# Optimization experiments

Measured on AMD Instinct MI355X. Metric: run time of the kernel, lower is better.

The kernel has to match this reference:

```python
import jax, jax.numpy as jnp
import numpy as np

N_SRC = 200000
N_DST = 50000
N_EDGES = 800000
IN_FEATS = 128
OUT_FEATS = 64


def setup_inputs() -> dict:
    key = jax.random.key(0)
    k1, k2, k3, k4 = jax.random.split(key, 4)
    x = jax.random.normal(k1, (N_SRC, IN_FEATS), dtype=jnp.float32)
    edge_src = jax.random.randint(k2, (N_EDGES,), 0, N_SRC, dtype=jnp.int64)
    edge_dst = jax.random.randint(k3, (N_EDGES,), 0, N_DST, dtype=jnp.int64)
    W = jax.random.normal(k4, (IN_FEATS, OUT_FEATS), dtype=jnp.float32) / np.sqrt(IN_FEATS)
    b = jnp.zeros((OUT_FEATS,), dtype=jnp.float32)
    return {"x": x, "edge_src": edge_src, "edge_dst": edge_dst, "W": W, "b": b, "n_dst": N_DST}


def reference(x, edge_src, edge_dst, W, b, n_dst):
    # DGL SAGEConv, aggregator_type='gcn'.
    # lin_before_mp = in_feats > out_feats (128 > 64) -> project before aggregation.
    h_src = x @ W                      # [n_src, out]
    h_dst = h_src[:n_dst]              # dst nodes are the first n_dst src nodes
    # sparse gather + segment reduce (SpMM): sum of projected neighbor feats per dst
    msgs = h_src[edge_src]             # [n_edges, out]
    neigh_sum = jax.ops.segment_sum(msgs, edge_dst, num_segments=n_dst)
    deg = jax.ops.segment_sum(jnp.ones_like(edge_dst, dtype=h_src.dtype),
                              edge_dst, num_segments=n_dst)  # in-degree per dst
    h = (neigh_sum + h_dst) / (deg + 1.0)[:, None]
    return h + b
```

## Files before the change

### kernel.cpp

```cpp
#include <hip/hip_runtime.h>
#include <hip/hip_bf16.h>

#define IN_F   128
#define OUT_F  64
#define CAP    96
#define NGB    512

typedef __attribute__((ext_vector_type(8))) short short8;
typedef __attribute__((ext_vector_type(4))) float floatx4;

__device__ inline unsigned short f32_to_bf16_rne(float f) {
    unsigned int u = __float_as_uint(f);
    unsigned int r = (u + 0x7FFFu + ((u >> 16) & 1u)) >> 16;
    return (unsigned short)r;
}
__device__ inline float bf16_to_f32(unsigned short u) {
    return __uint_as_float((unsigned int)u << 16);
}
__device__ inline unsigned int cvt_pk_bf16(float lo, float hi) {
    unsigned int r;
    asm volatile("v_cvt_pk_bf16_f32 %0, %1, %2" : "=v"(r) : "v"(lo), "v"(hi));
    return r;
}
__device__ __forceinline__ void async_copy16(const float* gsrc, float* ldst) {
    __builtin_amdgcn_global_load_lds(
        (const __attribute__((address_space(1))) unsigned int*)(const void*)gsrc,
        (__attribute__((address_space(3))) unsigned int*)(void*)ldst,
        16, 0, 0);
}

__global__ __launch_bounds__(256) void prep_w(const float* __restrict__ W,
                                              unsigned short* __restrict__ Wtg) {
    const int o = blockIdx.x * 256 + threadIdx.x;
    #pragma unroll
    for (int m = 0; m < 4; ++m) {
        const int idx = o + m * 2048;
        const int f = idx >> 9, r = idx & 511, l = r >> 3, j = r & 7;
        const int t = f >> 2, s = f & 3;
        const int k = 32 * s + 8 * (l >> 4) + j;
        const int c = 16 * t + (l & 15);
        Wtg[idx] = f32_to_bf16_rne(W[k * 64 + c]);
    }
}

__global__ __launch_bounds__(256) void bin_edges(const int* __restrict__ esrc,
                                                 const int* __restrict__ edst,
                                                 int* __restrict__ cnt,
                                                 int* __restrict__ elist,
                                                 int n_edges) {
    const int e = blockIdx.x * 256 + threadIdx.x;
    if (e < n_edges) {
        const int d = edst[e];
        const int slot = atomicAdd(&cnt[d], 1);
        if (slot < CAP) elist[(size_t)d * CAP + slot] = esrc[e];
    }
}

__global__ __launch_bounds__(256, 2) void gemm_xw(const float* __restrict__ x,
                                                  const unsigned short* __restrict__ Wtg,
                                                  unsigned short* __restrict__ h,
                                                  int nTiles) {
    __shared__ float xs[2][64 * 128];

    const int tid = threadIdx.x;
    const int lane = tid & 63;
    const int wave = tid >> 6;
    const int lrow = lane & 15;
    const int lkg  = lane >> 4;
    const int rx   = lrow & 7;

    short8 bf[4][4];
    #pragma unroll
    for (int f = 0; f < 16; ++f)
        (&bf[0][0])[f] = *reinterpret_cast<const short8*>(&Wtg[(f * 64 + lane) * 8]);
    asm volatile("s_waitcnt vmcnt(0)" ::: "memory");

    auto stage = [&](int buf, int tile) {
        const float* xt = x + (size_t)tile * 64 * IN_F;
        #pragma unroll
        for (int i = 0; i < 8; ++i) {
            const int j = (wave * 8 + i) * 64 + lane;
            const int row = j >> 5;
            const int c16 = (j & 31) ^ (row & 7);
            const float* src = xt + row * 128 + c16 * 4;
            float* dst = &xs[buf][(wave * 8 + i) * 256];
            async_copy16(src, dst);
        }
    };

    int cur = 0;
    int tile = blockIdx.x;
    if (tile < nTiles) stage(0, tile);

    for (; tile < nTiles; tile += NGB) {
        const int next = tile + NGB;
        if (next < nTiles) {
            stage(cur ^ 1, next);
            asm volatile("s_waitcnt vmcnt(8)" ::: "memory");
        } else {
            asm volatile("s_waitcnt vmcnt(0)" ::: "memory");
        }
        __builtin_amdgcn_sched_barrier(0);
        __builtin_amdgcn_s_barrier();

        const float* xt = &xs[cur][0];
        const int row = 16 * wave + lrow;
        short8 a[4];
        #pragma unroll
        for (int s = 0; s < 4; ++s) {
            const int ca = (8 * s + 2 * lkg) ^ rx;
            const int cb = (8 * s + 2 * lkg + 1) ^ rx;
            const float4 va = *reinterpret_cast<const float4*>(&xt[row * 128 + ca * 4]);
            const float4 vb = *reinterpret_cast<const float4*>(&xt[row * 128 + cb * 4]);
            union { unsigned int u[4]; short8 v; } cv;
            cv.u[0] = cvt_pk_bf16(va.x, va.y);
            cv.u[1] = cvt_pk_bf16(va.z, va.w);
            cv.u[2] = cvt_pk_bf16(vb.x, vb.y);
            cv.u[3] = cvt_pk_bf16(vb.z, vb.w);
            a[s] = cv.v;
        }

        floatx4 acc[4];
        #pragma unroll
        for (int t = 0; t < 4; ++t) acc[t] = (floatx4){0.f, 0.f, 0.f, 0.f};
        #pragma unroll
        for (int t = 0; t < 4; ++t)
            #pragma unroll
            for (int s = 0; s < 4; ++s)
                acc[t] = __builtin_amdgcn_mfma_f32_16x16x32_bf16(a[s], bf[t][s], acc[t], 0, 0, 0);

        unsigned short* hb = h + ((size_t)tile * 64 + 16 * wave) * OUT_F;
        #pragma unroll
        for (int t = 0; t < 4; ++t)
            #pragma unroll
            for (int r = 0; r < 4; ++r)
                hb[(size_t)(4 * lkg + r) * OUT_F + 16 * t + lrow] =
                    f32_to_bf16_rne(acc[t][r]);

        __builtin_amdgcn_s_barrier();
        cur ^= 1;
    }
}

__global__ __launch_bounds__(256) void gather_finalize(const unsigned short* __restrict__ h,
                                                       const int* __restrict__ cnt,
                                                       const int* __restrict__ elist,
                                                       const float* __restrict__ b,
                                                       float* __restrict__ out,
                                                       int n_dst) {
    const int lane = threadIdx.x & 63;
    const int d = blockIdx.x * 4 + (threadIdx.x >> 6);
    if (d >= n_dst) return;

    const int eq = lane >> 4;
    const int p  = lane & 15;

    const int cnt_d = cnt[d];
    const int m = min(cnt_d, CAP);
    const size_t ebase = (size_t)d * CAP;

    float4 acc = {0.f, 0.f, 0.f, 0.f};

    for (int base = 0; base < m; base += 64) {
        const int lim = min(64, m - base);
        const int sidx = (base + lane < m) ? elist[ebase + base + lane] : 0;
        for (int j = 0; j < lim; j += 4) {
            const int myj = j + eq;
            const bool valid = myj < lim;
            const int s = __shfl(sidx, valid ? myj : 0);
            const ushort4 v = *reinterpret_cast<const ushort4*>(&h[(size_t)s * OUT_F + 4 * p]);
            const float w = valid ? 1.0f : 0.0f;
            acc.x += w * bf16_to_f32(v.x);
            acc.y += w * bf16_to_f32(v.y);
            acc.z += w * bf16_to_f32(v.z);
            acc.w += w * bf16_to_f32(v.w);
        }
    }

    acc.x += __shfl_xor(acc.x, 32); acc.y += __shfl_xor(acc.y, 32);
    acc.z += __shfl_xor(acc.z, 32); acc.w += __shfl_xor(acc.w, 32);
    acc.x += __shfl_xor(acc.x, 16); acc.y += __shfl_xor(acc.y, 16);
    acc.z += __shfl_xor(acc.z, 16); acc.w += __shfl_xor(acc.w, 16);

    if (lane < 16) {
        const ushort4 hd = *reinterpret_cast<const ushort4*>(&h[(size_t)d * OUT_F + 4 * p]);
        const float4 bb = *reinterpret_cast<const float4*>(&b[4 * p]);
        const float inv = 1.0f / ((float)cnt_d + 1.0f);
        float4 o;
        o.x = (acc.x + bf16_to_f32(hd.x)) * inv + bb.x;
        o.y = (acc.y + bf16_to_f32(hd.y)) * inv + bb.y;
        o.z = (acc.z + bf16_to_f32(hd.z)) * inv + bb.z;
        o.w = (acc.w + bf16_to_f32(hd.w)) * inv + bb.w;
        *reinterpret_cast<float4*>(&out[(size_t)d * OUT_F + 4 * p]) = o;
    }
}

static inline size_t align256(size_t v) { return (v + 255) & ~(size_t)255; }

extern "C" void kernel_launch(void* const* d_in, const int* in_sizes, int n_in,
                              void* d_out, int out_size, void* d_ws, size_t ws_size,
                              hipStream_t stream) {
    const float* x    = (const float*)d_in[0];
    const int*   esrc = (const int*)d_in[1];
    const int*   edst = (const int*)d_in[2];
    const float* W    = (const float*)d_in[3];
    const float* b    = (const float*)d_in[4];

    const int n_rows  = in_sizes[0] / IN_F;
    const int n_edges = in_sizes[1];
    const int n_dst   = out_size / OUT_F;
    float* out = (float*)d_out;

    const size_t hBytes  = (size_t)n_rows * OUT_F * sizeof(unsigned short);
    const size_t cntOff  = align256(hBytes);
    const size_t elOff   = align256(cntOff + (size_t)n_dst * 4);
    const size_t wtOff   = align256(elOff + (size_t)n_dst * CAP * 4);
    const size_t needed  = wtOff + (size_t)IN_F * OUT_F * sizeof(unsigned short);

    unsigned short* h = (unsigned short*)d_ws;

    if (ws_size >= needed) {
        int* cnt             = (int*)((char*)d_ws + cntOff);
        int* elist           = (int*)((char*)d_ws + elOff);
        unsigned short* Wtg  = (unsigned short*)((char*)d_ws + wtOff);

        hipMemsetAsync(cnt, 0, (size_t)n_dst * 4, stream);

        prep_w<<<8, 256, 0, stream>>>(W, Wtg);

        const int eBlocks = (n_edges + 255) / 256;
        bin_edges<<<eBlocks, 256, 0, stream>>>(esrc, edst, cnt, elist, n_edges);

        const int nTiles = n_rows / 64;
        gemm_xw<<<NGB, 256, 0, stream>>>(x, Wtg, h, nTiles);

        const int gBlocks = (n_dst + 3) / 4;
        gather_finalize<<<gBlocks, 256, 0, stream>>>(h, cnt, elist, b, out, n_dst);
    } else {
        hipMemsetAsync(out, 0, (size_t)out_size * sizeof(float), stream);
    }
}
```

Measured before the change: 108.4 us.

## Fuse edge binning into GEMM kernel and split counters into front/back halves

Removes the separate bin_edges launch by running edge binning in a grid-stride loop at the end of the persistent GEMM kernel. Edges are split by parity into two counters that fill the per-destination slot list from the front and from the back, which halves contention on each atomic counter. The gather kernel reads the two ranges and uses the summed counts for the degree. The cost is a second counter array, and the binning still runs after each block's GEMM tiles rather than overlapping with them. The per-half cap of 48 can drop edges that the single cap of 96 would have kept when the two halves are uneven.

```diff
diff --git a/kernel.cpp b/kernel.cpp
--- a/kernel.cpp
+++ b/kernel.cpp
@@ -4,6 +4,7 @@
 #define IN_F   128
 #define OUT_F  64
 #define CAP    96
+#define HCAP   48
 #define NGB    512
 
 typedef __attribute__((ext_vector_type(8))) short short8;
@@ -43,23 +44,16 @@
     }
 }
 
-__global__ __launch_bounds__(256) void bin_edges(const int* __restrict__ esrc,
-                                                 const int* __restrict__ edst,
-                                                 int* __restrict__ cnt,
-                                                 int* __restrict__ elist,
-                                                 int n_edges) {
-    const int e = blockIdx.x * 256 + threadIdx.x;
-    if (e < n_edges) {
-        const int d = edst[e];
-        const int slot = atomicAdd(&cnt[d], 1);
-        if (slot < CAP) elist[(size_t)d * CAP + slot] = esrc[e];
-    }
-}
-
-__global__ __launch_bounds__(256, 2) void gemm_xw(const float* __restrict__ x,
-                                                  const unsigned short* __restrict__ Wtg,
-                                                  unsigned short* __restrict__ h,
-                                                  int nTiles) {
+__global__ __launch_bounds__(256, 2) void gemm_bin(const float* __restrict__ x,
+                                                   const unsigned short* __restrict__ Wtg,
+                                                   unsigned short* __restrict__ h,
+                                                   int nTiles,
+                                                   const int* __restrict__ esrc,
+                                                   const int* __restrict__ edst,
+                                                   int* __restrict__ cntF,
+                                                   int* __restrict__ cntB,
+                                                   int* __restrict__ elist,
+                                                   int n_edges) {
     __shared__ float xs[2][64 * 128];
 
     const int tid = threadIdx.x;
@@ -82,9 +76,7 @@
             const int j = (wave * 8 + i) * 64 + lane;
             const int row = j >> 5;
             const int c16 = (j & 31) ^ (row & 7);
-            const float* src = xt + row * 128 + c16 * 4;
-            float* dst = &xs[buf][(wave * 8 + i) * 256];
-            async_copy16(src, dst);
+            async_copy16(xt + row * 128 + c16 * 4, &xs[buf][(wave * 8 + i) * 256]);
         }
     };
 
@@ -140,10 +132,24 @@
         __builtin_amdgcn_s_barrier();
         cur ^= 1;
     }
+
+    const int gstride = NGB * 256;
+    for (int e = blockIdx.x * 256 + tid; e < n_edges; e += gstride) {
+        const int d = edst[e];
+        const int s = esrc[e];
+        if (e & 1) {
+            const int slot = atomicAdd(&cntB[d], 1);
+            if (slot < HCAP) elist[(size_t)d * CAP + (CAP - 1 - slot)] = s;
+        } else {
+            const int slot = atomicAdd(&cntF[d], 1);
+            if (slot < HCAP) elist[(size_t)d * CAP + slot] = s;
+        }
+    }
 }
 
 __global__ __launch_bounds__(256) void gather_finalize(const unsigned short* __restrict__ h,
-                                                       const int* __restrict__ cnt,
+                                                       const int* __restrict__ cntF,
+                                                       const int* __restrict__ cntB,
                                                        const int* __restrict__ elist,
                                                        const float* __restrict__ b,
                                                        float* __restrict__ out,
@@ -155,15 +161,20 @@
     const int eq = lane >> 4;
     const int p  = lane & 15;
 
-    const int cnt_d = cnt[d];
-    const int m = min(cnt_d, CAP);
+    const int cF = cntF[d];
+    const int cB = cntB[d];
+    const int m1 = min(cF, HCAP);
+    const int m2 = min(cB, HCAP);
+    const int m  = m1 + m2;
     const size_t ebase = (size_t)d * CAP;
 
     float4 acc = {0.f, 0.f, 0.f, 0.f};
 
     for (int base = 0; base < m; base += 64) {
         const int lim = min(64, m - base);
-        const int sidx = (base + lane < m) ? elist[ebase + base + lane] : 0;
+        const int pos = base + lane;
+        const int slot = (pos < m1) ? pos : (CAP - m2 + (pos - m1));
+        const int sidx = (pos < m) ? elist[ebase + slot] : 0;
         for (int j = 0; j < lim; j += 4) {
             const int myj = j + eq;
             const bool valid = myj < lim;
@@ -185,7 +196,7 @@
     if (lane < 16) {
         const ushort4 hd = *reinterpret_cast<const ushort4*>(&h[(size_t)d * OUT_F + 4 * p]);
         const float4 bb = *reinterpret_cast<const float4*>(&b[4 * p]);
-        const float inv = 1.0f / ((float)cnt_d + 1.0f);
+        const float inv = 1.0f / ((float)(cF + cB) + 1.0f);
         float4 o;
         o.x = (acc.x + bf16_to_f32(hd.x)) * inv + bb.x;
         o.y = (acc.y + bf16_to_f32(hd.y)) * inv + bb.y;
@@ -213,29 +224,28 @@
 
     const size_t hBytes  = (size_t)n_rows * OUT_F * sizeof(unsigned short);
     const size_t cntOff  = align256(hBytes);
-    const size_t elOff   = align256(cntOff + (size_t)n_dst * 4);
+    const size_t elOff   = align256(cntOff + 2 * (size_t)n_dst * 4);
     const size_t wtOff   = align256(elOff + (size_t)n_dst * CAP * 4);
     const size_t needed  = wtOff + (size_t)IN_F * OUT_F * sizeof(unsigned short);
 
     unsigned short* h = (unsigned short*)d_ws;
 
     if (ws_size >= needed) {
-        int* cnt             = (int*)((char*)d_ws + cntOff);
+        int* cntF            = (int*)((char*)d_ws + cntOff);
+        int* cntB            = cntF + n_dst;
         int* elist           = (int*)((char*)d_ws + elOff);
         unsigned short* Wtg  = (unsigned short*)((char*)d_ws + wtOff);
 
-        hipMemsetAsync(cnt, 0, (size_t)n_dst * 4, stream);
+        hipMemsetAsync(cntF, 0, 2 * (size_t)n_dst * 4, stream);
 
         prep_w<<<8, 256, 0, stream>>>(W, Wtg);
 
-        const int eBlocks = (n_edges + 255) / 256;
-        bin_edges<<<eBlocks, 256, 0, stream>>>(esrc, edst, cnt, elist, n_edges);
-
         const int nTiles = n_rows / 64;
-        gemm_xw<<<NGB, 256, 0, stream>>>(x, Wtg, h, nTiles);
+        gemm_bin<<<NGB, 256, 0, stream>>>(x, Wtg, h, nTiles,
+                                          esrc, edst, cntF, cntB, elist, n_edges);
 
         const int gBlocks = (n_dst + 3) / 4;
-        gather_finalize<<<gBlocks, 256, 0, stream>>>(h, cnt, elist, b, out, n_dst);
+        gather_finalize<<<gBlocks, 256, 0, stream>>>(h, cntF, cntB, elist, b, out, n_dst);
     } else {
         hipMemsetAsync(out, 0, (size_t)out_size * sizeof(float), stream);
     }
```

After: 124.1 us. 1.14x slower.
